# Kernel tuning notes

Measured on AMD Instinct MI355X. Metric: run time of the kernel, lower is better.

Reference implementation:

```python
import jax, jax.numpy as jnp
import numpy as np

H = 512          # hidden_size
DEPTH = 6        # number of tanh layers
N = 8192         # collocation points
DT = 0.1         # uniform time step
MIN_ALPHA = 0.6  # initial_params['min_alpha']


def _xavier(k, fi, fo):
    lim = np.sqrt(6.0 / (fi + fo))
    return jax.random.uniform(k, (fi, fo), minval=-lim, maxval=lim, dtype=jnp.float32)


def _raw(x):
    # inverse-softplus style init used by EpiPINN: raw = x + log(-expm1(-x))
    return jnp.array([x + np.log(-np.expm1(-x))], dtype=jnp.float32)


def setup_inputs() -> dict:
    key = jax.random.key(0)
    ks = jax.random.split(key, DEPTH + 2)
    W_in = _xavier(ks[0], 1, H)
    b_in = jnp.zeros((H,), jnp.float32)
    Wh = jnp.stack([_xavier(ks[1 + l], H, H) for l in range(DEPTH - 1)])  # [DEPTH-1,H,H]
    bh = jnp.zeros((DEPTH - 1, H), jnp.float32)
    W_out = _xavier(ks[DEPTH], H, 5)
    b_out = jnp.zeros((5,), jnp.float32)
    t = (jnp.arange(N, dtype=jnp.float32) * DT).reshape(N, 1)
    return {
        't': t,
        'W_in': W_in, 'b_in': b_in, 'Wh': Wh, 'bh': bh,
        'W_out': W_out, 'b_out': b_out,
        'raw_beta': _raw(0.3), 'raw_sigma': _raw(0.2),
        'raw_gamma': _raw(0.1), 'raw_mu': _raw(0.05),
        'z_alpha': jnp.array([0.0], dtype=jnp.float32),
    }


def _forward_all(t, W_in, b_in, Wh, bh, W_out, b_out,
                 raw_beta, raw_sigma, raw_gamma, raw_mu, z_alpha):
    # --- PINN MLP: 1 -> H (tanh) x DEPTH -> 5, softmax over components ---
    h = jnp.tanh(t @ W_in + b_in)
    for l in range(Wh.shape[0]):  # static small loop over layers
        h = jnp.tanh(h @ Wh[l] + bh[l])
    y = jax.nn.softmax(h @ W_out + b_out, axis=1)  # [n,5]

    alpha = MIN_ALPHA + (1.0 - MIN_ALPHA) * jax.nn.sigmoid(z_alpha[0])
    beta = jax.nn.softplus(raw_beta[0])
    sigma = jax.nn.softplus(raw_sigma[0])
    gamma = jax.nn.softplus(raw_gamma[0])
    mu = jax.nn.softplus(raw_mu[0])

    # --- Caputo L1 fractional derivative for all 5 components at once ---
    n = y.shape[0]
    dpsi = y[1:] - y[:-1]  # [n-1,5] first differences
    rs = jnp.arange(n - 1, dtype=y.dtype)
    rs_safe = jnp.where(rs == 0, 1.0, rs)  # avoid 0**x grad nan; value unchanged
    ws = (rs + 1.0) ** (1.0 - alpha) - jnp.where(rs == 0, 0.0, rs_safe ** (1.0 - alpha))
    C = DT ** (-alpha) / jnp.exp(jax.lax.lgamma(2.0 - alpha))
    ii = jnp.arange(n - 1)
    idx = ii[:, None] - ii[None, :]
    A = jnp.where(idx >= 0, ws[jnp.clip(idx, 0)], 0.0)  # lower-triangular Toeplitz [n-1,n-1]
    dfrac = jnp.concatenate([jnp.zeros((1, 5), y.dtype), C * (A @ dpsi)], axis=0)  # [n,5]

    # --- SEIRD right-hand side and physics residual ---
    s, e, i, r, d = (y[:, k:k + 1] for k in range(5))
    living = 1.0 - d
    inf_term = beta * s * i / living
    f = jnp.concatenate([
        -inf_term,
        inf_term - sigma * e,
        sigma * e - (gamma + mu) * i,
        gamma * i,
        mu * i,
    ], axis=1)  # [n,5]
    return jnp.mean((dfrac - f) ** 2)


def reference(t, W_in, b_in, Wh, bh, W_out, b_out,
              raw_beta, raw_sigma, raw_gamma, raw_mu, z_alpha):
    return _forward_all(t, W_in, b_in, Wh, bh, W_out, b_out,
                        raw_beta, raw_sigma, raw_gamma, raw_mu, z_alpha)
```

## Files before the change

### kernel.cpp

```cpp
#include <hip/hip_runtime.h>
#include <math.h>

typedef short short8v __attribute__((ext_vector_type(8)));
typedef float float4v __attribute__((ext_vector_type(4)));

#define N_PTS 8192
#define HDIM  512
#define NHID  5
#define KSTR  1024
#define NCH   16

#define OFF_XA    0ull
#define OFF_XB    16777216ull
#define OFF_WT    33554432ull
#define OFF_Y     38797312ull
#define OFF_PART  39157760ull
#define OFF_BPART 41779200ull

__device__ __forceinline__ unsigned short f2bf(float x) {
  unsigned u = __builtin_bit_cast(unsigned, x);
  u += 0x7FFFu + ((u >> 16) & 1u);
  return (unsigned short)(u >> 16);
}
__device__ __forceinline__ float bf2f(unsigned short h) {
  unsigned u = ((unsigned)h) << 16;
  return __builtin_bit_cast(float, u);
}

#define GLOAD16(gsrc, ldst) \
  __builtin_amdgcn_global_load_lds( \
      (const __attribute__((address_space(1))) void*)(gsrc), \
      (__attribute__((address_space(3))) void*)(ldst), 16, 0, 0)

__global__ void prep_kernel(const float* __restrict__ Wh,
                            unsigned short* __restrict__ WT,
                            const float* __restrict__ t,
                            const float* __restrict__ Win,
                            const float* __restrict__ bin,
                            unsigned short* __restrict__ X) {
  int bid = blockIdx.x;
  if (bid < 1280) {
    __shared__ float tile[32][33];
    int kb = bid & 15, n0 = ((bid >> 4) & 15) * 32, l = bid >> 8;
    int j = threadIdx.x & 31, i8 = threadIdx.x >> 5;
    const float* W = Wh + (size_t)l * HDIM * HDIM;
#pragma unroll
    for (int q = 0; q < 4; ++q)
      tile[i8 + 8 * q][j] = W[(size_t)(kb * 32 + i8 + 8 * q) * HDIM + n0 + j];
    __syncthreads();
#pragma unroll
    for (int q = 0; q < 4; ++q) {
      int n = n0 + i8 + 8 * q;
      float v = tile[j][i8 + 8 * q];
      unsigned short h = f2bf(v);
      unsigned short lo = f2bf(v - bf2f(h));
      size_t o = ((size_t)l * HDIM + n) * KSTR + kb * 64 + j;
      WT[o] = h; WT[o + 32] = lo;
    }
  } else {
    int gid = (bid - 1280) * 256 + threadIdx.x;
    int row = gid >> 7;
    int jq  = (gid & 127) << 2;
    float tv = t[row];
    float4 w = *(const float4*)(Win + jq);
    float4 b = *(const float4*)(bin + jq);
    float v[4];
    v[0] = tanhf(tv * w.x + b.x); v[1] = tanhf(tv * w.y + b.y);
    v[2] = tanhf(tv * w.z + b.z); v[3] = tanhf(tv * w.w + b.w);
    ushort4 h4, l4;
    h4.x = f2bf(v[0]); l4.x = f2bf(v[0] - bf2f(h4.x));
    h4.y = f2bf(v[1]); l4.y = f2bf(v[1] - bf2f(h4.y));
    h4.z = f2bf(v[2]); l4.z = f2bf(v[2] - bf2f(h4.z));
    h4.w = f2bf(v[3]); l4.w = f2bf(v[3] - bf2f(h4.w));
    size_t o = (size_t)row * KSTR + (jq >> 5) * 64 + (jq & 31);
    *(ushort4*)(X + o) = h4;
    *(ushort4*)(X + o + 32) = l4;
  }
}

__global__ __launch_bounds__(512, 4) void gemm_split_kernel(
    const unsigned short* __restrict__ A,
    const unsigned short* __restrict__ Bt,
    const float* __restrict__ bias,
    unsigned short* __restrict__ C) {
  __shared__ __align__(16) short lds[3][12288];
  const int tid = threadIdx.x;
  const int lane = tid & 63, w = tid >> 6;
  const int wr = w >> 2, wc = w & 3;
  const int r0 = blockIdx.x * 64, c0 = blockIdx.y * 128;
  const int rl = lane & 15, kgrp = lane >> 4;

  float4v acc[2][2];
#pragma unroll
  for (int i = 0; i < 2; ++i)
#pragma unroll
    for (int j = 0; j < 2; ++j) acc[i][j] = (float4v){0.f, 0.f, 0.f, 0.f};

  auto stage = [&](int b, int kt) {
    const int kbase = kt * 64;
    {
      int c = tid;
      int row = c >> 3, m = c & 7;
      int gs = m ^ (row & 7);
      GLOAD16(A + (size_t)(r0 + row) * KSTR + kbase + gs * 8,
              &lds[b][(w * 64) * 8]);
    }
#pragma unroll
    for (int i = 0; i < 2; ++i) {
      int c = i * 512 + tid;
      int col = c >> 3, m = c & 7;
      int gs = m ^ (col & 7);
      GLOAD16(Bt + (size_t)(c0 + col) * KSTR + kbase + gs * 8,
              &lds[b][4096 + (i * 512 + w * 64) * 8]);
    }
  };

  stage(0, 0);
  stage(1, 1);
  asm volatile("s_waitcnt vmcnt(3)" ::: "memory");
  __builtin_amdgcn_s_barrier();
  asm volatile("" ::: "memory");

#pragma unroll 1
  for (int kt = 0; kt < 16; ++kt) {
    if (kt < 14) stage((kt + 2) % 3, kt + 2);
    const short* bufc = lds[kt % 3];
    short8v ahi[2], alo[2], bhi[2], blo[2];
#pragma unroll
    for (int mi = 0; mi < 2; ++mi) {
      int row = wr * 32 + mi * 16 + rl;
      int sh = kgrp ^ (row & 7);
      int sl = (kgrp + 4) ^ (row & 7);
      ahi[mi] = *(const short8v*)&bufc[row * 64 + sh * 8];
      alo[mi] = *(const short8v*)&bufc[row * 64 + sl * 8];
    }
#pragma unroll
    for (int ni = 0; ni < 2; ++ni) {
      int col = wc * 32 + ni * 16 + rl;
      int sh = kgrp ^ (col & 7);
      int sl = (kgrp + 4) ^ (col & 7);
      bhi[ni] = *(const short8v*)&bufc[4096 + col * 64 + sh * 8];
      blo[ni] = *(const short8v*)&bufc[4096 + col * 64 + sl * 8];
    }
    __builtin_amdgcn_s_setprio(1);
#pragma unroll
    for (int mi = 0; mi < 2; ++mi)
#pragma unroll
      for (int ni = 0; ni < 2; ++ni)
        acc[mi][ni] = __builtin_amdgcn_mfma_f32_16x16x32_bf16(ahi[mi], bhi[ni], acc[mi][ni], 0, 0, 0);
#pragma unroll
    for (int mi = 0; mi < 2; ++mi)
#pragma unroll
      for (int ni = 0; ni < 2; ++ni)
        acc[mi][ni] = __builtin_amdgcn_mfma_f32_16x16x32_bf16(ahi[mi], blo[ni], acc[mi][ni], 0, 0, 0);
#pragma unroll
    for (int mi = 0; mi < 2; ++mi)
#pragma unroll
      for (int ni = 0; ni < 2; ++ni)
        acc[mi][ni] = __builtin_amdgcn_mfma_f32_16x16x32_bf16(alo[mi], bhi[ni], acc[mi][ni], 0, 0, 0);
    __builtin_amdgcn_s_setprio(0);
    if (kt < 15) {
      if (kt < 14) asm volatile("s_waitcnt vmcnt(3)" ::: "memory");
      else         asm volatile("s_waitcnt vmcnt(0)" ::: "memory");
      __builtin_amdgcn_s_barrier();
      asm volatile("" ::: "memory");
    }
  }

  float bcol[2];
#pragma unroll
  for (int ni = 0; ni < 2; ++ni) bcol[ni] = bias[c0 + wc * 32 + ni * 16 + rl];
#pragma unroll
  for (int mi = 0; mi < 2; ++mi)
#pragma unroll
    for (int ni = 0; ni < 2; ++ni)
#pragma unroll
      for (int r = 0; r < 4; ++r) {
        int row = r0 + wr * 32 + mi * 16 + kgrp * 4 + r;
        int col = c0 + wc * 32 + ni * 16 + rl;
        float v = tanhf(acc[mi][ni][r] + bcol[ni]);
        unsigned short h = f2bf(v);
        unsigned short lo = f2bf(v - bf2f(h));
        size_t o = (size_t)row * KSTR + (col >> 5) * 64 + (col & 31);
        C[o] = h; C[o + 32] = lo;
      }
}

__global__ void outlayer_kernel(const unsigned short* __restrict__ X,
                                const float* __restrict__ Wout,
                                const float* __restrict__ bout,
                                float* __restrict__ y) {
  int wid  = threadIdx.x >> 6;
  int lane = threadIdx.x & 63;
  int row  = blockIdx.x * 4 + wid;
  size_t o = (size_t)row * KSTR + (lane >> 2) * 64 + (lane & 3) * 8;
  short8v hv = *(const short8v*)(X + o);
  short8v lv = *(const short8v*)(X + o + 32);
  const float* wrp = Wout + lane * 40;
  float acc[5] = {0.f, 0.f, 0.f, 0.f, 0.f};
#pragma unroll
  for (int e = 0; e < 8; ++e) {
    float h = bf2f((unsigned short)hv[e]) + bf2f((unsigned short)lv[e]);
#pragma unroll
    for (int c = 0; c < 5; ++c) acc[c] += h * wrp[e * 5 + c];
  }
#pragma unroll
  for (int c = 0; c < 5; ++c)
    for (int off = 32; off; off >>= 1) acc[c] += __shfl_down(acc[c], off);
  if (lane == 0) {
    float l[5], m = -1e30f;
#pragma unroll
    for (int c = 0; c < 5; ++c) { l[c] = acc[c] + bout[c]; m = fmaxf(m, l[c]); }
    float s = 0.f;
#pragma unroll
    for (int c = 0; c < 5; ++c) { l[c] = expf(l[c] - m); s += l[c]; }
    float inv = 1.f / s;
#pragma unroll
    for (int c = 0; c < 5; ++c) y[row * 5 + c] = l[c] * inv;
  }
}

__global__ __launch_bounds__(256) void conv_kernel(
    const float* __restrict__ y, const float* __restrict__ za,
    float* __restrict__ part) {
  __shared__ float dps[256][8];
  __shared__ float wsl[512];
  int tid = threadIdx.x;
  int r0  = blockIdx.x * 256;
  int ch  = blockIdx.y;
  int r   = r0 + tid;
  float acc[5] = {0.f, 0.f, 0.f, 0.f, 0.f};

  double z = (double)za[0];
  double alpha = 0.6 + 0.4 / (1.0 + exp(-z));
  double p = 1.0 - alpha;

  for (int t4 = 0; t4 < 2; ++t4) {
    int j0 = ch * 512 + t4 * 256;
    if (j0 > r0 + 254) break;
    __syncthreads();
    {
      int jr = j0 + tid;
      if (jr <= N_PTS - 2) {
        const float* y0 = y + (size_t)jr * 5;
        dps[tid][0] = y0[5] - y0[0]; dps[tid][1] = y0[6] - y0[1];
        dps[tid][2] = y0[7] - y0[2]; dps[tid][3] = y0[8] - y0[3];
        dps[tid][4] = y0[9] - y0[4];
      } else {
        dps[tid][0] = dps[tid][1] = dps[tid][2] = dps[tid][3] = dps[tid][4] = 0.f;
      }
    }
    int base = r0 - j0 - 256;
#pragma unroll
    for (int s = 0; s < 2; ++s) {
      int i = tid + s * 256;
      int src = base + i;
      float wv = 0.f;
      if (src >= 0 && src < N_PTS - 1) {
        double ww = pow((double)src + 1.0, p) -
                    (src == 0 ? 0.0 : pow((double)src, p));
        wv = (float)ww;
      }
      wsl[i] = wv;
    }
    __syncthreads();
    int widx = tid + 255;
#pragma unroll 4
    for (int jj = 0; jj < 256; ++jj) {
      float w = wsl[widx - jj];
      float4 d4 = *(const float4*)&dps[jj][0];
      float d5 = dps[jj][4];
      acc[0] += w * d4.x; acc[1] += w * d4.y; acc[2] += w * d4.z;
      acc[3] += w * d4.w; acc[4] += w * d5;
    }
  }
  float* pp = part + ((size_t)ch * N_PTS + r) * 5;
  pp[0] = acc[0]; pp[1] = acc[1]; pp[2] = acc[2]; pp[3] = acc[3]; pp[4] = acc[4];
}

__device__ __forceinline__ float softplusf_(float x) {
  return x > 20.f ? x : log1pf(expf(x));
}

__global__ void combine_kernel(const float* __restrict__ y,
                               const float* __restrict__ part,
                               const float* __restrict__ rb, const float* __restrict__ rs,
                               const float* __restrict__ rg, const float* __restrict__ rm,
                               const float* __restrict__ za,
                               float* __restrict__ bpart) {
  __shared__ float red[128];
  int tid = threadIdx.x;
  int row = blockIdx.x * 128 + tid;

  float beta  = softplusf_(rb[0]);
  float sigma = softplusf_(rs[0]);
  float gamma = softplusf_(rg[0]);
  float mu    = softplusf_(rm[0]);
  double z = (double)za[0];
  double alpha = 0.6 + 0.4 / (1.0 + exp(-z));
  float C = (float)(pow(0.1, -alpha) / tgamma(2.0 - alpha));

  float df[5];
  if (row == 0) {
    df[0] = df[1] = df[2] = df[3] = df[4] = 0.f;
  } else {
#pragma unroll
    for (int c = 0; c < 5; ++c) {
      float s = 0.f;
#pragma unroll
      for (int ch = 0; ch < NCH; ++ch)
        s += part[((size_t)ch * N_PTS + row) * 5 + c];
      df[c] = C * s;
    }
  }
  float yv[5];
#pragma unroll
  for (int c = 0; c < 5; ++c) yv[c] = y[row * 5 + c];
  float living = 1.f - yv[4];
  float inf_t = beta * yv[0] * yv[2] / living;
  float f[5];
  f[0] = -inf_t;
  f[1] = inf_t - sigma * yv[1];
  f[2] = sigma * yv[1] - (gamma + mu) * yv[2];
  f[3] = gamma * yv[2];
  f[4] = mu * yv[2];
  float s = 0.f;
#pragma unroll
  for (int c = 0; c < 5; ++c) { float d = df[c] - f[c]; s += d * d; }

  red[tid] = s;
  __syncthreads();
  for (int off = 64; off; off >>= 1) {
    if (tid < off) red[tid] += red[tid + off];
    __syncthreads();
  }
  if (tid == 0) bpart[blockIdx.x] = red[0];
}

__global__ void finish_kernel(const float* __restrict__ bpart, float* __restrict__ out) {
  if (threadIdx.x == 0) {
    float s = 0.f;
    for (int i = 0; i < 64; ++i) s += bpart[i];
    out[0] = s / (float)(N_PTS * 5);
  }
}

extern "C" void kernel_launch(void* const* d_in, const int* in_sizes, int n_in,
                              void* d_out, int out_size, void* d_ws, size_t ws_size,
                              hipStream_t stream) {
  const float* t     = (const float*)d_in[0];
  const float* W_in  = (const float*)d_in[1];
  const float* b_in  = (const float*)d_in[2];
  const float* Wh    = (const float*)d_in[3];
  const float* bh    = (const float*)d_in[4];
  const float* W_out = (const float*)d_in[5];
  const float* b_out = (const float*)d_in[6];
  const float* rbta  = (const float*)d_in[7];
  const float* rsig  = (const float*)d_in[8];
  const float* rgam  = (const float*)d_in[9];
  const float* rmu   = (const float*)d_in[10];
  const float* zalp  = (const float*)d_in[11];

  char* wsb = (char*)d_ws;
  unsigned short* XA = (unsigned short*)(wsb + OFF_XA);
  unsigned short* XB = (unsigned short*)(wsb + OFF_XB);
  unsigned short* WT = (unsigned short*)(wsb + OFF_WT);
  float* y     = (float*)(wsb + OFF_Y);
  float* part  = (float*)(wsb + OFF_PART);
  float* bpart = (float*)(wsb + OFF_BPART);
  float* out   = (float*)d_out;

  prep_kernel<<<5376, 256, 0, stream>>>(Wh, WT, t, W_in, b_in, XA);

  for (int l = 0; l < NHID; ++l) {
    const unsigned short* in = (l & 1) ? XB : XA;
    unsigned short*      oub = (l & 1) ? XA : XB;
    gemm_split_kernel<<<dim3(N_PTS / 64, HDIM / 128), 512, 0, stream>>>(
        in, WT + (size_t)l * HDIM * KSTR, bh + (size_t)l * HDIM, oub);
  }

  outlayer_kernel<<<N_PTS / 4, 256, 0, stream>>>(XB, W_out, b_out, y);

  conv_kernel<<<dim3(N_PTS / 256, NCH), 256, 0, stream>>>(y, zalp, part);

  combine_kernel<<<N_PTS / 128, 128, 0, stream>>>(y, part, rbta, rsig, rgam, rmu,
                                                  zalp, bpart);
  finish_kernel<<<1, 64, 0, stream>>>(bpart, out);
  (void)in_sizes; (void)n_in; (void)out_size; (void)ws_size;
}
```

Measured before the change: 132.9 us.

## Replace LDS-staged split-bf16 GEMM with direct global-to-register fragment loads

```diff
diff --git a/kernel.cpp b/kernel.cpp
--- a/kernel.cpp
+++ b/kernel.cpp
@@ -7,8 +7,11 @@
 #define N_PTS 8192
 #define HDIM  512
 #define NHID  5
-#define KSTR  1024
 #define NCH   16
+
+#define A_KT  524288
+#define A_H   262144
+#define B_LKT 16384
 
 #define OFF_XA    0ull
 #define OFF_XB    16777216ull
@@ -27,38 +30,32 @@
   return __builtin_bit_cast(float, u);
 }
 
-#define GLOAD16(gsrc, ldst) \
-  __builtin_amdgcn_global_load_lds( \
-      (const __attribute__((address_space(1))) void*)(gsrc), \
-      (__attribute__((address_space(3))) void*)(ldst), 16, 0, 0)
-
 __global__ void prep_kernel(const float* __restrict__ Wh,
-                            unsigned short* __restrict__ WT,
+                            unsigned short* __restrict__ WB,
                             const float* __restrict__ t,
                             const float* __restrict__ Win,
                             const float* __restrict__ bin,
                             unsigned short* __restrict__ X) {
   int bid = blockIdx.x;
-  if (bid < 1280) {
-    __shared__ float tile[32][33];
-    int kb = bid & 15, n0 = ((bid >> 4) & 15) * 32, l = bid >> 8;
-    int j = threadIdx.x & 31, i8 = threadIdx.x >> 5;
-    const float* W = Wh + (size_t)l * HDIM * HDIM;
-#pragma unroll
-    for (int q = 0; q < 4; ++q)
-      tile[i8 + 8 * q][j] = W[(size_t)(kb * 32 + i8 + 8 * q) * HDIM + n0 + j];
-    __syncthreads();
-#pragma unroll
-    for (int q = 0; q < 4; ++q) {
-      int n = n0 + i8 + 8 * q;
-      float v = tile[j][i8 + 8 * q];
-      unsigned short h = f2bf(v);
-      unsigned short lo = f2bf(v - bf2f(h));
-      size_t o = ((size_t)l * HDIM + n) * KSTR + kb * 64 + j;
-      WT[o] = h; WT[o + 32] = lo;
+  int tid = threadIdx.x;
+  if (bid < 80) {
+    int l = bid >> 4, kt = bid & 15;
+    const float* W = Wh + (size_t)l * HDIM * HDIM + (size_t)kt * 32 * HDIM;
+    size_t ob = (size_t)((l * 16 + kt) * 2) * B_LKT;
+#pragma unroll 1
+    for (int kk = 0; kk < 32; ++kk) {
+#pragma unroll
+      for (int s = 0; s < 2; ++s) {
+        int n = s * 256 + tid;
+        float v = W[kk * HDIM + n];
+        unsigned short h = f2bf(v);
+        unsigned short lo = f2bf(v - bf2f(h));
+        size_t o = ob + (size_t)n * 32 + kk;
+        WB[o] = h; WB[o + B_LKT] = lo;
+      }
     }
   } else {
-    int gid = (bid - 1280) * 256 + threadIdx.x;
+    int gid = (bid - 80) * 256 + tid;
     int row = gid >> 7;
     int jq  = (gid & 127) << 2;
     float tv = t[row];
@@ -72,118 +69,104 @@
     h4.y = f2bf(v[1]); l4.y = f2bf(v[1] - bf2f(h4.y));
     h4.z = f2bf(v[2]); l4.z = f2bf(v[2] - bf2f(h4.z));
     h4.w = f2bf(v[3]); l4.w = f2bf(v[3] - bf2f(h4.w));
-    size_t o = (size_t)row * KSTR + (jq >> 5) * 64 + (jq & 31);
+    size_t o = (size_t)(jq >> 5) * A_KT + (size_t)row * 32 +
+               (((jq & 31) >> 3) * 8) + (jq & 7);
     *(ushort4*)(X + o) = h4;
-    *(ushort4*)(X + o + 32) = l4;
-  }
-}
-
-__global__ __launch_bounds__(512, 4) void gemm_split_kernel(
+    *(ushort4*)(X + o + A_H) = l4;
+  }
+}
+
+struct Frags { short8v ah[2], al[2], bh[2], bl[2]; };
+
+__device__ __forceinline__ Frags loadf(const unsigned short* __restrict__ A,
+                                       const unsigned short* __restrict__ WB,
+                                       int kt, const int* aoff, const int* boff) {
+  Frags f;
+#pragma unroll
+  for (int mi = 0; mi < 2; ++mi) {
+    f.ah[mi] = *(const short8v*)(A + (size_t)kt * A_KT + aoff[mi]);
+    f.al[mi] = *(const short8v*)(A + (size_t)kt * A_KT + A_H + aoff[mi]);
+  }
+#pragma unroll
+  for (int ni = 0; ni < 2; ++ni) {
+    f.bh[ni] = *(const short8v*)(WB + (size_t)kt * 2 * B_LKT + boff[ni]);
+    f.bl[ni] = *(const short8v*)(WB + (size_t)kt * 2 * B_LKT + B_LKT + boff[ni]);
+  }
+  return f;
+}
+
+__device__ __forceinline__ void comp(const Frags& f, float4v acc[2][2]) {
+#pragma unroll
+  for (int mi = 0; mi < 2; ++mi)
+#pragma unroll
+    for (int ni = 0; ni < 2; ++ni)
+      acc[mi][ni] = __builtin_amdgcn_mfma_f32_16x16x32_bf16(
+          f.ah[mi], f.bh[ni], acc[mi][ni], 0, 0, 0);
+#pragma unroll
+  for (int mi = 0; mi < 2; ++mi)
+#pragma unroll
+    for (int ni = 0; ni < 2; ++ni)
+      acc[mi][ni] = __builtin_amdgcn_mfma_f32_16x16x32_bf16(
+          f.ah[mi], f.bl[ni], acc[mi][ni], 0, 0, 0);
+#pragma unroll
+  for (int mi = 0; mi < 2; ++mi)
+#pragma unroll
+    for (int ni = 0; ni < 2; ++ni)
+      acc[mi][ni] = __builtin_amdgcn_mfma_f32_16x16x32_bf16(
+          f.al[mi], f.bh[ni], acc[mi][ni], 0, 0, 0);
+}
+
+__global__ __launch_bounds__(512, 4) void gemm_direct_kernel(
     const unsigned short* __restrict__ A,
-    const unsigned short* __restrict__ Bt,
+    const unsigned short* __restrict__ WB,
     const float* __restrict__ bias,
     unsigned short* __restrict__ C) {
-  __shared__ __align__(16) short lds[3][12288];
   const int tid = threadIdx.x;
   const int lane = tid & 63, w = tid >> 6;
   const int wr = w >> 2, wc = w & 3;
   const int r0 = blockIdx.x * 64, c0 = blockIdx.y * 128;
   const int rl = lane & 15, kgrp = lane >> 4;
 
+  int aoff[2], boff[2];
+#pragma unroll
+  for (int mi = 0; mi < 2; ++mi)
+    aoff[mi] = (r0 + wr * 32 + mi * 16 + rl) * 32 + kgrp * 8;
+#pragma unroll
+  for (int ni = 0; ni < 2; ++ni)
+    boff[ni] = (c0 + wc * 32 + ni * 16 + rl) * 32 + kgrp * 8;
+
   float4v acc[2][2];
 #pragma unroll
   for (int i = 0; i < 2; ++i)
 #pragma unroll
     for (int j = 0; j < 2; ++j) acc[i][j] = (float4v){0.f, 0.f, 0.f, 0.f};
 
-  auto stage = [&](int b, int kt) {
-    const int kbase = kt * 64;
-    {
-      int c = tid;
-      int row = c >> 3, m = c & 7;
-      int gs = m ^ (row & 7);
-      GLOAD16(A + (size_t)(r0 + row) * KSTR + kbase + gs * 8,
-              &lds[b][(w * 64) * 8]);
-    }
-#pragma unroll
-    for (int i = 0; i < 2; ++i) {
-      int c = i * 512 + tid;
-      int col = c >> 3, m = c & 7;
-      int gs = m ^ (col & 7);
-      GLOAD16(Bt + (size_t)(c0 + col) * KSTR + kbase + gs * 8,
-              &lds[b][4096 + (i * 512 + w * 64) * 8]);
-    }
-  };
-
-  stage(0, 0);
-  stage(1, 1);
-  asm volatile("s_waitcnt vmcnt(3)" ::: "memory");
-  __builtin_amdgcn_s_barrier();
-  asm volatile("" ::: "memory");
-
+  Frags f0 = loadf(A, WB, 0, aoff, boff);
 #pragma unroll 1
-  for (int kt = 0; kt < 16; ++kt) {
-    if (kt < 14) stage((kt + 2) % 3, kt + 2);
-    const short* bufc = lds[kt % 3];
-    short8v ahi[2], alo[2], bhi[2], blo[2];
-#pragma unroll
-    for (int mi = 0; mi < 2; ++mi) {
-      int row = wr * 32 + mi * 16 + rl;
-      int sh = kgrp ^ (row & 7);
-      int sl = (kgrp + 4) ^ (row & 7);
-      ahi[mi] = *(const short8v*)&bufc[row * 64 + sh * 8];
-      alo[mi] = *(const short8v*)&bufc[row * 64 + sl * 8];
-    }
-#pragma unroll
-    for (int ni = 0; ni < 2; ++ni) {
-      int col = wc * 32 + ni * 16 + rl;
-      int sh = kgrp ^ (col & 7);
-      int sl = (kgrp + 4) ^ (col & 7);
-      bhi[ni] = *(const short8v*)&bufc[4096 + col * 64 + sh * 8];
-      blo[ni] = *(const short8v*)&bufc[4096 + col * 64 + sl * 8];
-    }
-    __builtin_amdgcn_s_setprio(1);
+  for (int kt = 0; kt < 16; kt += 2) {
+    Frags f1 = loadf(A, WB, kt + 1, aoff, boff);
+    comp(f0, acc);
+    if (kt + 2 < 16) f0 = loadf(A, WB, kt + 2, aoff, boff);
+    comp(f1, acc);
+  }
+
+#pragma unroll
+  for (int ni = 0; ni < 2; ++ni) {
+    int col = c0 + wc * 32 + ni * 16 + rl;
+    float bc = bias[col];
+    size_t och = (size_t)((col >> 5) * 2) * A_H + ((col & 31) >> 3) * 8 + (col & 7);
 #pragma unroll
     for (int mi = 0; mi < 2; ++mi)
-#pragma unroll
-      for (int ni = 0; ni < 2; ++ni)
-        acc[mi][ni] = __builtin_amdgcn_mfma_f32_16x16x32_bf16(ahi[mi], bhi[ni], acc[mi][ni], 0, 0, 0);
-#pragma unroll
-    for (int mi = 0; mi < 2; ++mi)
-#pragma unroll
-      for (int ni = 0; ni < 2; ++ni)
-        acc[mi][ni] = __builtin_amdgcn_mfma_f32_16x16x32_bf16(ahi[mi], blo[ni], acc[mi][ni], 0, 0, 0);
-#pragma unroll
-    for (int mi = 0; mi < 2; ++mi)
-#pragma unroll
-      for (int ni = 0; ni < 2; ++ni)
-        acc[mi][ni] = __builtin_amdgcn_mfma_f32_16x16x32_bf16(alo[mi], bhi[ni], acc[mi][ni], 0, 0, 0);
-    __builtin_amdgcn_s_setprio(0);
-    if (kt < 15) {
-      if (kt < 14) asm volatile("s_waitcnt vmcnt(3)" ::: "memory");
-      else         asm volatile("s_waitcnt vmcnt(0)" ::: "memory");
-      __builtin_amdgcn_s_barrier();
-      asm volatile("" ::: "memory");
-    }
-  }
-
-  float bcol[2];
-#pragma unroll
-  for (int ni = 0; ni < 2; ++ni) bcol[ni] = bias[c0 + wc * 32 + ni * 16 + rl];
-#pragma unroll
-  for (int mi = 0; mi < 2; ++mi)
-#pragma unroll
-    for (int ni = 0; ni < 2; ++ni)
 #pragma unroll
       for (int r = 0; r < 4; ++r) {
         int row = r0 + wr * 32 + mi * 16 + kgrp * 4 + r;
-        int col = c0 + wc * 32 + ni * 16 + rl;
-        float v = tanhf(acc[mi][ni][r] + bcol[ni]);
+        float v = tanhf(acc[mi][ni][r] + bc);
         unsigned short h = f2bf(v);
         unsigned short lo = f2bf(v - bf2f(h));
-        size_t o = (size_t)row * KSTR + (col >> 5) * 64 + (col & 31);
-        C[o] = h; C[o + 32] = lo;
+        size_t o = och + (size_t)row * 32;
+        C[o] = h; C[o + A_H] = lo;
       }
+  }
 }
 
 __global__ void outlayer_kernel(const unsigned short* __restrict__ X,
@@ -193,9 +176,9 @@
   int wid  = threadIdx.x >> 6;
   int lane = threadIdx.x & 63;
   int row  = blockIdx.x * 4 + wid;
-  size_t o = (size_t)row * KSTR + (lane >> 2) * 64 + (lane & 3) * 8;
+  size_t o = (size_t)(lane >> 2) * A_KT + (size_t)row * 32 + (lane & 3) * 8;
   short8v hv = *(const short8v*)(X + o);
-  short8v lv = *(const short8v*)(X + o + 32);
+  short8v lv = *(const short8v*)(X + o + A_H);
   const float* wrp = Wout + lane * 40;
   float acc[5] = {0.f, 0.f, 0.f, 0.f, 0.f};
 #pragma unroll
@@ -364,19 +347,19 @@
   char* wsb = (char*)d_ws;
   unsigned short* XA = (unsigned short*)(wsb + OFF_XA);
   unsigned short* XB = (unsigned short*)(wsb + OFF_XB);
-  unsigned short* WT = (unsigned short*)(wsb + OFF_WT);
+  unsigned short* WB = (unsigned short*)(wsb + OFF_WT);
   float* y     = (float*)(wsb + OFF_Y);
   float* part  = (float*)(wsb + OFF_PART);
   float* bpart = (float*)(wsb + OFF_BPART);
   float* out   = (float*)d_out;
 
-  prep_kernel<<<5376, 256, 0, stream>>>(Wh, WT, t, W_in, b_in, XA);
+  prep_kernel<<<4176, 256, 0, stream>>>(Wh, WB, t, W_in, b_in, XA);
 
   for (int l = 0; l < NHID; ++l) {
     const unsigned short* in = (l & 1) ? XB : XA;
     unsigned short*      oub = (l & 1) ? XA : XB;
-    gemm_split_kernel<<<dim3(N_PTS / 64, HDIM / 128), 512, 0, stream>>>(
-        in, WT + (size_t)l * HDIM * KSTR, bh + (size_t)l * HDIM, oub);
+    gemm_direct_kernel<<<dim3(N_PTS / 64, HDIM / 128), 512, 0, stream>>>(
+        in, WB + (size_t)l * 16 * 2 * B_LKT, bh + (size_t)l * HDIM, oub);
   }
 
   outlayer_kernel<<<N_PTS / 4, 256, 0, stream>>>(XB, W_out, b_out, y);
```

After: 229.3 us. 72.5% more time.
